# Performance work log

Hardware: AMD Instinct MI355X
Metric: run time of the kernel (lower is better)

## Reference

```python
import jax, jax.numpy as jnp
import numpy as np

D_MODEL = 32
N_HEADS = 4
D_K = 8
D_V = 8
LN_EPS = 1e-5
MASK_FILL = -1.0e9


def _layernorm(x, eps=LN_EPS):
    # torch.nn.LayerNorm with default affine params (gamma=1, beta=0)
    mu = jnp.mean(x, axis=-1, keepdims=True)
    var = jnp.var(x, axis=-1, keepdims=True)  # biased, matches torch
    return (x - mu) * jax.lax.rsqrt(var + eps)


def setup_inputs() -> dict:
    key = jax.random.key(0)
    ks = jax.random.split(key, 12)
    B, S = 8, 2048
    w = 1.0 / np.float32(np.sqrt(D_MODEL))
    return {
        "input_Q": jax.random.normal(ks[0], (B, S, D_MODEL), dtype=jnp.float32),
        "input_K": jax.random.normal(ks[1], (B, S, D_MODEL), dtype=jnp.float32),
        "input_V": jax.random.normal(ks[2], (B, S, D_MODEL), dtype=jnp.float32),
        "attn_mask": jax.random.randint(ks[3], (B, S, S), 0, 2).astype(jnp.bool_),
        "W_Q": jax.random.normal(ks[4], (D_MODEL, D_K * N_HEADS), dtype=jnp.float32) * w,
        "b_Q": jax.random.normal(ks[5], (D_K * N_HEADS,), dtype=jnp.float32) * 0.02,
        "W_K": jax.random.normal(ks[6], (D_MODEL, D_K * N_HEADS), dtype=jnp.float32) * w,
        "b_K": jax.random.normal(ks[7], (D_K * N_HEADS,), dtype=jnp.float32) * 0.02,
        "W_V": jax.random.normal(ks[8], (D_MODEL, D_V * N_HEADS), dtype=jnp.float32) * w,
        "b_V": jax.random.normal(ks[9], (D_V * N_HEADS,), dtype=jnp.float32) * 0.02,
        "W_O": jax.random.normal(ks[10], (D_V * N_HEADS, D_MODEL), dtype=jnp.float32) * w,
        "b_O": jax.random.normal(ks[11], (D_MODEL,), dtype=jnp.float32) * 0.02,
    }


def reference(input_Q, input_K, input_V, attn_mask, W_Q, b_Q, W_K, b_K, W_V, b_V, W_O, b_O):
    B, S, _ = input_Q.shape
    residual = input_Q
    # projections -> [B, H, S, d_head]
    Q = (input_Q @ W_Q + b_Q).reshape(B, S, N_HEADS, D_K).transpose(0, 2, 1, 3)
    K = (input_K @ W_K + b_K).reshape(B, S, N_HEADS, D_K).transpose(0, 2, 1, 3)
    V = (input_V @ W_V + b_V).reshape(B, S, N_HEADS, D_V).transpose(0, 2, 1, 3)
    scale = 1.0 / jnp.sqrt(jnp.asarray(D_K, dtype=Q.dtype))
    scores = jnp.einsum("bhqd,bhkd->bhqk", Q, K) * scale  # [B,H,S,S]
    scores = jnp.where(attn_mask[:, None, :, :], jnp.asarray(MASK_FILL, scores.dtype), scores)
    attn_ratio = jax.nn.softmax(scores, axis=-1)
    ctx = jnp.einsum("bhqk,bhkd->bhqd", attn_ratio, V)  # [B,H,S,Dv]
    self_attn = ctx.transpose(0, 2, 1, 3).reshape(B, S, N_HEADS * D_V)
    attn_output = self_attn @ W_O + b_O
    return (_layernorm(attn_output + residual), self_attn)
```

## Files before the change

### kernel.cpp

```cpp
#include <hip/hip_runtime.h>
#include <math.h>

#define D_MODEL 32
#define S_LEN   2048
#define B_SZ    8
#define NTOK    (B_SZ * S_LEN)
#define LN_EPS  1e-5f
#define LOG2E   1.44269504088896340736f
#define QK_SCALE 0.35355339059327373f
#define PROJ_BLKS (NTOK / 8)

typedef __attribute__((ext_vector_type(8)))  short    short8b;
typedef __attribute__((ext_vector_type(4)))  short    short4b;
typedef __attribute__((ext_vector_type(4)))  unsigned uint4v;
typedef __attribute__((ext_vector_type(16))) float    f32x16;

__device__ __forceinline__ unsigned short f2bf(float f) {
    unsigned u = __builtin_bit_cast(unsigned, f);
    unsigned r = (u + 0x7FFFu + ((u >> 16) & 1u)) >> 16;
    return (unsigned short)r;
}
__device__ __forceinline__ float bf2f(unsigned short h) {
    return __builtin_bit_cast(float, (unsigned)h << 16);
}
__device__ __forceinline__ unsigned cvtpk_bf16(float lo, float hi) {
    unsigned r;
    asm("v_cvt_pk_bf16_f32 %0, %1, %2" : "=v"(r) : "v"(lo), "v"(hi));
    return r;
}


__global__ __launch_bounds__(256) void prep_kernel(
    const float* __restrict__ xQ, const float* __restrict__ xK,
    const float* __restrict__ xV,
    const float* __restrict__ WQ, const float* __restrict__ bQ,
    const float* __restrict__ WK, const float* __restrict__ bK,
    const float* __restrict__ WV, const float* __restrict__ bV,
    unsigned short* __restrict__ QHC, unsigned short* __restrict__ QLC,
    unsigned short* __restrict__ KC,  unsigned short* __restrict__ VC)
{
    int bid = blockIdx.x;
    int t   = threadIdx.x;

    int which = bid / PROJ_BLKS;
    int xb    = bid - which * PROJ_BLKS;
    const float* x; const float* W; const float* bias; float scale;
    if (which == 0)      { x = xQ; W = WQ; bias = bQ; scale = QK_SCALE * LOG2E; }
    else if (which == 1) { x = xK; W = WK; bias = bK; scale = 1.0f; }
    else                 { x = xV; W = WV; bias = bV; scale = 1.0f; }

    __shared__ float xs[8][32];
    __shared__ float Ws[32][32];
    long base = (long)xb * 256;
    xs[t >> 5][t & 31] = x[base + t];
#pragma unroll
    for (int i = 0; i < 4; ++i) {
        int f = i * 256 + t;
        Ws[f >> 5][f & 31] = W[f];
    }
    __syncthreads();
    int r = t >> 5, j = t & 31;
    float acc = bias[j];
#pragma unroll
    for (int i = 0; i < 32; ++i) acc = fmaf(xs[r][i], Ws[i][j], acc);
    acc *= scale;

    long tok = (long)xb * 8 + r;
    long b   = tok >> 11;
    long ti  = tok & (S_LEN - 1);
    int  ch  = (int)(ti >> 5), kq = (int)(ti & 31);
    int  h   = j >> 3, d = j & 7;

    if (which == 0) {
        size_t qi = ((((size_t)b * 64 + ch) * 4 + h) * 32 + kq) * 8 + d;
        unsigned short hv = f2bf(acc);
        QHC[qi] = hv;
        QLC[qi] = f2bf(acc - bf2f(hv));
    } else if (which == 1) {
        size_t ki = (((((size_t)b * 64 + ch) * 4 + h) * 2 + 0) * 32 + kq) * 8 + d;
        unsigned short hv = f2bf(acc);
        KC[ki]       = hv;
        KC[ki + 256] = f2bf(acc - bf2f(hv));
    } else {
        size_t vi = (((size_t)b * 64 + ch) * 4 + h) * 256 + (size_t)d * 32 + kq;
        VC[vi] = f2bf(acc);
    }
}

__global__ __launch_bounds__(512, 4) void attn_fused_kernel(
    const unsigned short* __restrict__ QHC, const unsigned short* __restrict__ QLC,
    const unsigned short* __restrict__ KC,  const unsigned short* __restrict__ VC,
    const void* __restrict__ mask,
    const float* __restrict__ WO, const float* __restrict__ bO,
    const float* __restrict__ resid,
    float* __restrict__ sa_out, float* __restrict__ out0)
{
    constexpr int SEGLEN = 1024;
    constexpr int NPT    = SEGLEN / 64;
    __shared__ unsigned long long mpk[2][2][32][5];
    __shared__ float ctx_lds[2][32][33];
    __shared__ float l_lds[2][32][4];
    __shared__ float sa_lds[32][33];
    __shared__ float Ws[32][32];

    int raw  = blockIdx.x;
    int cid  = (raw & 7) * 64 + (raw >> 3);
    int b    = cid >> 6;
    int qt   = cid & 63;
    int tid  = threadIdx.x;
    int w    = tid >> 6;
    int h    = w & 3;
    int seg  = w >> 2;
    int lane = tid & 63;
    int q    = lane & 31;
    int half = lane >> 5;
    int tok0 = qt * 32;
    long tokbase = (long)b * S_LEN + tok0;
    long tokq    = tokbase + q;
    int k0   = seg * SEGLEN;
    int ch0  = k0 >> 5;

#pragma unroll
    for (int i = 0; i < 2; ++i) {
        int f = i * 512 + tid;
        Ws[f >> 5][f & 31] = WO[f];
    }

    int probe = ((const int*)mask)[lane];
    bool is32 = (__ballot((probe & ~0xFF) == 0) == ~0ULL);

    auto pack_group = [&](int g, int buf) {
#pragma unroll
        for (int i = 0; i < 4; ++i) {
            int r = (w << 2) + i;
            if (is32) {
                const int4* rp = (const int4*)((const int*)mask
                                               + (tokbase + r) * (long)S_LEN);
#pragma unroll
                for (int s2 = 0; s2 < 2; ++s2) {
                    int4 v = rp[s2 * 256 + g * 64 + lane];
                    unsigned long long b0 = __ballot(v.x != 0);
                    unsigned long long b1 = __ballot(v.y != 0);
                    unsigned long long b2 = __ballot(v.z != 0);
                    unsigned long long b3 = __ballot(v.w != 0);
                    if (lane == 0) {
                        mpk[buf][s2][r][0] = b0; mpk[buf][s2][r][1] = b1;
                        mpk[buf][s2][r][2] = b2; mpk[buf][s2][r][3] = b3;
                    }
                }
            } else {
                const int* rp = (const int*)((const unsigned char*)mask
                                             + (tokbase + r) * (long)S_LEN);
#pragma unroll
                for (int s2 = 0; s2 < 2; ++s2) {
                    int v = rp[s2 * 256 + g * 64 + lane];
                    unsigned long long b0 = __ballot((v & 0x000000FF) != 0);
                    unsigned long long b1 = __ballot((v & 0x0000FF00) != 0);
                    unsigned long long b2 = __ballot((v & 0x00FF0000) != 0);
                    unsigned long long b3 = __ballot((v & 0xFF000000u) != 0);
                    if (lane == 0) {
                        mpk[buf][s2][r][0] = b0; mpk[buf][s2][r][1] = b1;
                        mpk[buf][s2][r][2] = b2; mpk[buf][s2][r][3] = b3;
                    }
                }
            }
        }
    };

    f32x16 zero16;
#pragma unroll
    for (int i = 0; i < 16; ++i) zero16[i] = 0.0f;

    short ovv = (q == 8) ? (short)0x3F80 : (short)0;
    short8b ovf;
#pragma unroll
    for (int i = 0; i < 8; ++i) ovf[i] = ovv;

    size_t qoff = ((((size_t)b * 64 + qt) * 4 + h) * 32 + q) * 8;
    short8b qhf = *(const short8b*)(QHC + qoff);
    short8b qlf = *(const short8b*)(QLC + qoff);
    f32x16 cpv = zero16;

    const unsigned short* Kb0 = KC + (((size_t)b * 64) * 4 + h) * 512
                                   + (size_t)half * 256 + (size_t)q * 8;
    const unsigned short* Vb0 = VC + (((size_t)b * 64) * 4 + h) * 256
                                   + (size_t)q * 32 + half * 4;

    short8b kfA = *(const short8b*)(Kb0 + (size_t)ch0 * 2048);
    short8b kfB = *(const short8b*)(Kb0 + (size_t)(ch0 + 1) * 2048);
    short8b vf1c, vf2c;
    if (q < 8) {
        const unsigned short* vr = Vb0 + (size_t)ch0 * 1024;
        short4b a0 = *(const short4b*)(vr);
        short4b a1 = *(const short4b*)(vr + 8);
        short4b a2 = *(const short4b*)(vr + 16);
        short4b a3 = *(const short4b*)(vr + 24);
        vf1c = __builtin_shufflevector(a0, a1, 0, 1, 2, 3, 4, 5, 6, 7);
        vf2c = __builtin_shufflevector(a2, a3, 0, 1, 2, 3, 4, 5, 6, 7);
    } else { vf1c = ovf; vf2c = ovf; }

    pack_group(0, 0);
    __syncthreads();

#pragma unroll 1
    for (int g = 0; g < 4; ++g) {
        int cur = g & 1;

        if (g + 1 < 4) pack_group(g + 1, cur ^ 1);

        unsigned long long mg[4];
        mg[0] = mpk[cur][seg][q][0];
        mg[1] = mpk[cur][seg][q][1];
        mg[2] = mpk[cur][seg][q][2];
        mg[3] = mpk[cur][seg][q][3];

#pragma unroll 1
        for (int p = 0; p < 4; ++p) {
            int pa  = g * 4 + p;
            int chA = ch0 + 2 * pa;
            int chB = chA + 1;

            short8b kfA_n = kfA, kfB_n = kfB;
            if (pa + 1 < NPT) {
                kfA_n = *(const short8b*)(Kb0 + (size_t)(chA + 2) * 2048);
                kfB_n = *(const short8b*)(Kb0 + (size_t)(chB + 2) * 2048);
            }

            unsigned shA = (unsigned)(p * 16 + half);
            unsigned nA[4], nB[4];
#pragma unroll
            for (int c = 0; c < 4; ++c) {
                nA[c] = (unsigned)(mg[c] >> shA);
                nB[c] = (unsigned)(mg[c] >> (shA + 8u));
            }

            __builtin_amdgcn_s_setprio(1);
            f32x16 accA = __builtin_amdgcn_mfma_f32_32x32x16_bf16(kfA, qhf, zero16, 0, 0, 0);
            f32x16 accB = __builtin_amdgcn_mfma_f32_32x32x16_bf16(kfB, qhf, zero16, 0, 0, 0);
            accA = __builtin_amdgcn_mfma_f32_32x32x16_bf16(kfA, qlf, accA, 0, 0, 0);
            accB = __builtin_amdgcn_mfma_f32_32x32x16_bf16(kfB, qlf, accB, 0, 0, 0);
            __builtin_amdgcn_s_setprio(0);

            short8b vf1n, vf2n;
            if (q < 8) {
                const unsigned short* vr = Vb0 + (size_t)chB * 1024;
                short4b a0 = *(const short4b*)(vr);
                short4b a1 = *(const short4b*)(vr + 8);
                short4b a2 = *(const short4b*)(vr + 16);
                short4b a3 = *(const short4b*)(vr + 24);
                vf1n = __builtin_shufflevector(a0, a1, 0, 1, 2, 3, 4, 5, 6, 7);
                vf2n = __builtin_shufflevector(a2, a3, 0, 1, 2, 3, 4, 5, 6, 7);
            } else { vf1n = ovf; vf2n = ovf; }

            {
                unsigned pr[8];
#pragma unroll
                for (int j = 0; j < 8; ++j) {
                    const int c0 = (2 * j) & 3, c1 = (2 * j + 1) & 3;
                    const int s  = 2 * (j >> 1);
                    float p0 = ((nA[c0] >> s) & 1u) ? 0.0f
                             : __builtin_amdgcn_exp2f(accA[2 * j]);
                    float p1 = ((nA[c1] >> s) & 1u) ? 0.0f
                             : __builtin_amdgcn_exp2f(accA[2 * j + 1]);
                    pr[j] = cvtpk_bf16(p0, p1);
                }
                uint4v t1, t2;
                t1.x = pr[0]; t1.y = pr[1]; t1.z = pr[2]; t1.w = pr[3];
                t2.x = pr[4]; t2.y = pr[5]; t2.z = pr[6]; t2.w = pr[7];
                short8b pfa = __builtin_bit_cast(short8b, t1);
                short8b pfb = __builtin_bit_cast(short8b, t2);

                __builtin_amdgcn_s_setprio(1);
                cpv = __builtin_amdgcn_mfma_f32_32x32x16_bf16(vf1c, pfa, cpv, 0, 0, 0);
                cpv = __builtin_amdgcn_mfma_f32_32x32x16_bf16(vf2c, pfb, cpv, 0, 0, 0);
                __builtin_amdgcn_s_setprio(0);
            }

            short8b vf1nn, vf2nn;
            if (pa + 1 < NPT && q < 8) {
                const unsigned short* vr = Vb0 + (size_t)(chA + 2) * 1024;
                short4b a0 = *(const short4b*)(vr);
                short4b a1 = *(const short4b*)(vr + 8);
                short4b a2 = *(const short4b*)(vr + 16);
                short4b a3 = *(const short4b*)(vr + 24);
                vf1nn = __builtin_shufflevector(a0, a1, 0, 1, 2, 3, 4, 5, 6, 7);
                vf2nn = __builtin_shufflevector(a2, a3, 0, 1, 2, 3, 4, 5, 6, 7);
            } else { vf1nn = ovf; vf2nn = ovf; }

            {
                unsigned pr[8];
#pragma unroll
                for (int j = 0; j < 8; ++j) {
                    const int c0 = (2 * j) & 3, c1 = (2 * j + 1) & 3;
                    const int s  = 2 * (j >> 1);
                    float p0 = ((nB[c0] >> s) & 1u) ? 0.0f
                             : __builtin_amdgcn_exp2f(accB[2 * j]);
                    float p1 = ((nB[c1] >> s) & 1u) ? 0.0f
                             : __builtin_amdgcn_exp2f(accB[2 * j + 1]);
                    pr[j] = cvtpk_bf16(p0, p1);
                }
                uint4v t1, t2;
                t1.x = pr[0]; t1.y = pr[1]; t1.z = pr[2]; t1.w = pr[3];
                t2.x = pr[4]; t2.y = pr[5]; t2.z = pr[6]; t2.w = pr[7];
                short8b pfa = __builtin_bit_cast(short8b, t1);
                short8b pfb = __builtin_bit_cast(short8b, t2);

                __builtin_amdgcn_s_setprio(1);
                cpv = __builtin_amdgcn_mfma_f32_32x32x16_bf16(vf1n, pfa, cpv, 0, 0, 0);
                cpv = __builtin_amdgcn_mfma_f32_32x32x16_bf16(vf2n, pfb, cpv, 0, 0, 0);
                __builtin_amdgcn_s_setprio(0);
            }

            kfA = kfA_n;
            kfB = kfB_n;
            vf1c = vf1nn;
            vf2c = vf2nn;
        }

        __syncthreads();
    }

    ctx_lds[seg][q][h * 8 + half * 4 + 0] = cpv[0];
    ctx_lds[seg][q][h * 8 + half * 4 + 1] = cpv[1];
    ctx_lds[seg][q][h * 8 + half * 4 + 2] = cpv[2];
    ctx_lds[seg][q][h * 8 + half * 4 + 3] = cpv[3];
    if (half == 0) l_lds[seg][q][h] = cpv[4];
    __syncthreads();

    int r = (tid >> 5) & 15;
    int j = tid & 31;
#pragma unroll
    for (int pass = 0; pass < 2; ++pass) {
        int tok = pass * 16 + r;
        float L  = l_lds[0][tok][j >> 3] + l_lds[1][tok][j >> 3];
        float cx = ctx_lds[0][tok][j] + ctx_lds[1][tok][j];
        float sa = cx / L;
        sa_lds[tok][j] = sa;
        sa_out[(tokbase + tok) * 32 + j] = sa;
    }
    __syncthreads();

#pragma unroll
    for (int pass = 0; pass < 2; ++pass) {
        int tok = pass * 16 + r;
        long grow = (tokbase + tok) * 32;
        float y = bO[j] + resid[grow + j];
#pragma unroll
        for (int i = 0; i < 32; ++i) y = fmaf(sa_lds[tok][i], Ws[i][j], y);

        float sum = y;
#pragma unroll
        for (int o = 16; o >= 1; o >>= 1) sum += __shfl_xor(sum, o, 32);
        float mu = sum * (1.0f / 32.0f);
        float d  = y - mu;
        float sq = d * d;
#pragma unroll
        for (int o = 16; o >= 1; o >>= 1) sq += __shfl_xor(sq, o, 32);
        float var = sq * (1.0f / 32.0f);
        out0[grow + j] = d * rsqrtf(var + LN_EPS);
    }
}

extern "C" void kernel_launch(void* const* d_in, const int* in_sizes, int n_in,
                              void* d_out, int out_size, void* d_ws, size_t ws_size,
                              hipStream_t stream)
{
    const float* inQ = (const float*)d_in[0];
    const float* inK = (const float*)d_in[1];
    const float* inV = (const float*)d_in[2];
    const void*  mask = d_in[3];
    const float* WQ = (const float*)d_in[4];
    const float* bQ = (const float*)d_in[5];
    const float* WK = (const float*)d_in[6];
    const float* bK = (const float*)d_in[7];
    const float* WV = (const float*)d_in[8];
    const float* bV = (const float*)d_in[9];
    const float* WO = (const float*)d_in[10];
    const float* bO = (const float*)d_in[11];

    float* out0 = (float*)d_out;
    float* sa   = (float*)d_out + (long)NTOK * 32;

    char* ws = (char*)d_ws;
    unsigned short* QHC = (unsigned short*)(ws + 256);
    unsigned short* QLC = QHC + (size_t)NTOK * 32;
    unsigned short* KC  = QLC + (size_t)NTOK * 32;
    unsigned short* VC  = KC  + (size_t)NTOK * 64;

    prep_kernel<<<3 * PROJ_BLKS, 256, 0, stream>>>(
        inQ, inK, inV, WQ, bQ, WK, bK, WV, bV, QHC, QLC, KC, VC);

    attn_fused_kernel<<<B_SZ * 64, 512, 0, stream>>>(
        QHC, QLC, KC, VC, mask, WO, bO, inQ, sa, out0);
}
```

Baseline: 61.50 us.

## Split mask prefetch into issue/commit and unroll inner pair loop

Mask loads for the next group are now issued into registers at the start of a group. The ballot-and-LDS packing is deferred until after two of the four pair iterations, so global load latency overlaps with MFMA and exp work instead of stalling before compute. The inner loop over four pairs is also fully unrolled through a macro. This raises register pressure from the eight held int4 mask values and the larger unrolled code, which may reduce occupancy.

```diff
diff --git a/kernel.cpp b/kernel.cpp
--- a/kernel.cpp
+++ b/kernel.cpp
@@ -116,7 +116,6 @@
     int half = lane >> 5;
     int tok0 = qt * 32;
     long tokbase = (long)b * S_LEN + tok0;
-    long tokq    = tokbase + q;
     int k0   = seg * SEGLEN;
     int ch0  = k0 >> 5;
 
@@ -129,43 +128,56 @@
     int probe = ((const int*)mask)[lane];
     bool is32 = (__ballot((probe & ~0xFF) == 0) == ~0ULL);
 
-    auto pack_group = [&](int g, int buf) {
-#pragma unroll
-        for (int i = 0; i < 4; ++i) {
-            int r = (w << 2) + i;
-            if (is32) {
-                const int4* rp = (const int4*)((const int*)mask
-                                               + (tokbase + r) * (long)S_LEN);
-#pragma unroll
-                for (int s2 = 0; s2 < 2; ++s2) {
-                    int4 v = rp[s2 * 256 + g * 64 + lane];
-                    unsigned long long b0 = __ballot(v.x != 0);
-                    unsigned long long b1 = __ballot(v.y != 0);
-                    unsigned long long b2 = __ballot(v.z != 0);
-                    unsigned long long b3 = __ballot(v.w != 0);
-                    if (lane == 0) {
-                        mpk[buf][s2][r][0] = b0; mpk[buf][s2][r][1] = b1;
-                        mpk[buf][s2][r][2] = b2; mpk[buf][s2][r][3] = b3;
-                    }
-                }
-            } else {
-                const int* rp = (const int*)((const unsigned char*)mask
-                                             + (tokbase + r) * (long)S_LEN);
-#pragma unroll
-                for (int s2 = 0; s2 < 2; ++s2) {
-                    int v = rp[s2 * 256 + g * 64 + lane];
-                    unsigned long long b0 = __ballot((v & 0x000000FF) != 0);
-                    unsigned long long b1 = __ballot((v & 0x0000FF00) != 0);
-                    unsigned long long b2 = __ballot((v & 0x00FF0000) != 0);
-                    unsigned long long b3 = __ballot((v & 0xFF000000u) != 0);
-                    if (lane == 0) {
-                        mpk[buf][s2][r][0] = b0; mpk[buf][s2][r][1] = b1;
-                        mpk[buf][s2][r][2] = b2; mpk[buf][s2][r][3] = b3;
-                    }
-                }
-            }
-        }
-    };
+    long rb = tokbase + (w << 2);
+    const int4* r32_0 = (const int4*)((const int*)mask + (rb + 0) * (long)S_LEN);
+    const int4* r32_1 = (const int4*)((const int*)mask + (rb + 1) * (long)S_LEN);
+    const int4* r32_2 = (const int4*)((const int*)mask + (rb + 2) * (long)S_LEN);
+    const int4* r32_3 = (const int4*)((const int*)mask + (rb + 3) * (long)S_LEN);
+    const int* r8_0 = (const int*)((const unsigned char*)mask + (rb + 0) * (long)S_LEN);
+    const int* r8_1 = (const int*)((const unsigned char*)mask + (rb + 1) * (long)S_LEN);
+    const int* r8_2 = (const int*)((const unsigned char*)mask + (rb + 2) * (long)S_LEN);
+    const int* r8_3 = (const int*)((const unsigned char*)mask + (rb + 3) * (long)S_LEN);
+
+    int4 m0_0, m0_1, m1_0, m1_1, m2_0, m2_1, m3_0, m3_1;
+
+#define MASK_ISSUE(G)                                                        \
+    if (is32) {                                                              \
+        m0_0 = r32_0[(G) * 64 + lane]; m0_1 = r32_0[256 + (G) * 64 + lane];  \
+        m1_0 = r32_1[(G) * 64 + lane]; m1_1 = r32_1[256 + (G) * 64 + lane];  \
+        m2_0 = r32_2[(G) * 64 + lane]; m2_1 = r32_2[256 + (G) * 64 + lane];  \
+        m3_0 = r32_3[(G) * 64 + lane]; m3_1 = r32_3[256 + (G) * 64 + lane];  \
+    } else {                                                                 \
+        m0_0.x = r8_0[(G) * 64 + lane]; m0_1.x = r8_0[256 + (G) * 64 + lane];\
+        m1_0.x = r8_1[(G) * 64 + lane]; m1_1.x = r8_1[256 + (G) * 64 + lane];\
+        m2_0.x = r8_2[(G) * 64 + lane]; m2_1.x = r8_2[256 + (G) * 64 + lane];\
+        m3_0.x = r8_3[(G) * 64 + lane]; m3_1.x = r8_3[256 + (G) * 64 + lane];\
+    }
+
+#define CMT1(MV, RI, S2, BUF)                                                \
+    {                                                                        \
+        unsigned long long c0, c1, c2, c3;                                   \
+        if (is32) {                                                          \
+            c0 = __ballot((MV).x != 0); c1 = __ballot((MV).y != 0);          \
+            c2 = __ballot((MV).z != 0); c3 = __ballot((MV).w != 0);          \
+        } else {                                                             \
+            c0 = __ballot(((MV).x & 0x000000FF) != 0);                       \
+            c1 = __ballot(((MV).x & 0x0000FF00) != 0);                       \
+            c2 = __ballot(((MV).x & 0x00FF0000) != 0);                       \
+            c3 = __ballot(((MV).x & 0xFF000000u) != 0);                      \
+        }                                                                    \
+        if (lane == 0) {                                                     \
+            mpk[BUF][S2][(w << 2) + (RI)][0] = c0;                           \
+            mpk[BUF][S2][(w << 2) + (RI)][1] = c1;                           \
+            mpk[BUF][S2][(w << 2) + (RI)][2] = c2;                           \
+            mpk[BUF][S2][(w << 2) + (RI)][3] = c3;                           \
+        }                                                                    \
+    }
+
+#define MASK_COMMIT(BUF)                                                     \
+    CMT1(m0_0, 0, 0, BUF) CMT1(m0_1, 0, 1, BUF)                              \
+    CMT1(m1_0, 1, 0, BUF) CMT1(m1_1, 1, 1, BUF)                              \
+    CMT1(m2_0, 2, 0, BUF) CMT1(m2_1, 2, 1, BUF)                              \
+    CMT1(m3_0, 3, 0, BUF) CMT1(m3_1, 3, 1, BUF)
 
     f32x16 zero16;
 #pragma unroll
@@ -199,14 +211,105 @@
         vf2c = __builtin_shufflevector(a2, a3, 0, 1, 2, 3, 4, 5, 6, 7);
     } else { vf1c = ovf; vf2c = ovf; }
 
-    pack_group(0, 0);
+    MASK_ISSUE(0)
+    MASK_COMMIT(0)
     __syncthreads();
+
+#define PAIR_BODY(G, PP)                                                     \
+    {                                                                        \
+        int pa  = (G) * 4 + (PP);                                            \
+        int chA = ch0 + 2 * pa;                                              \
+        int chB = chA + 1;                                                   \
+        short8b kfA_n = kfA, kfB_n = kfB;                                    \
+        if (pa + 1 < NPT) {                                                  \
+            kfA_n = *(const short8b*)(Kb0 + (size_t)(chA + 2) * 2048);       \
+            kfB_n = *(const short8b*)(Kb0 + (size_t)(chB + 2) * 2048);       \
+        }                                                                    \
+        unsigned shA = (unsigned)((PP) * 16 + half);                         \
+        unsigned nA[4], nB[4];                                               \
+        _Pragma("unroll")                                                    \
+        for (int c = 0; c < 4; ++c) {                                        \
+            nA[c] = (unsigned)(mg[c] >> shA);                                \
+            nB[c] = (unsigned)(mg[c] >> (shA + 8u));                         \
+        }                                                                    \
+        __builtin_amdgcn_s_setprio(1);                                       \
+        f32x16 accA = __builtin_amdgcn_mfma_f32_32x32x16_bf16(kfA, qhf, zero16, 0, 0, 0); \
+        f32x16 accB = __builtin_amdgcn_mfma_f32_32x32x16_bf16(kfB, qhf, zero16, 0, 0, 0); \
+        accA = __builtin_amdgcn_mfma_f32_32x32x16_bf16(kfA, qlf, accA, 0, 0, 0); \
+        accB = __builtin_amdgcn_mfma_f32_32x32x16_bf16(kfB, qlf, accB, 0, 0, 0); \
+        __builtin_amdgcn_s_setprio(0);                                       \
+        short8b vf1n, vf2n;                                                  \
+        if (q < 8) {                                                         \
+            const unsigned short* vr = Vb0 + (size_t)chB * 1024;             \
+            short4b a0 = *(const short4b*)(vr);                              \
+            short4b a1 = *(const short4b*)(vr + 8);                          \
+            short4b a2 = *(const short4b*)(vr + 16);                         \
+            short4b a3 = *(const short4b*)(vr + 24);                         \
+            vf1n = __builtin_shufflevector(a0, a1, 0, 1, 2, 3, 4, 5, 6, 7);  \
+            vf2n = __builtin_shufflevector(a2, a3, 0, 1, 2, 3, 4, 5, 6, 7);  \
+        } else { vf1n = ovf; vf2n = ovf; }                                   \
+        {                                                                    \
+            unsigned pr[8];                                                  \
+            _Pragma("unroll")                                                \
+            for (int j2 = 0; j2 < 8; ++j2) {                                 \
+                const int c0 = (2 * j2) & 3, c1 = (2 * j2 + 1) & 3;          \
+                const int s  = 2 * (j2 >> 1);                                \
+                float p0 = ((nA[c0] >> s) & 1u) ? 0.0f                       \
+                         : __builtin_amdgcn_exp2f(accA[2 * j2]);             \
+                float p1 = ((nA[c1] >> s) & 1u) ? 0.0f                       \
+                         : __builtin_amdgcn_exp2f(accA[2 * j2 + 1]);         \
+                pr[j2] = cvtpk_bf16(p0, p1);                                 \
+            }                                                                \
+            uint4v t1, t2;                                                   \
+            t1.x = pr[0]; t1.y = pr[1]; t1.z = pr[2]; t1.w = pr[3];          \
+            t2.x = pr[4]; t2.y = pr[5]; t2.z = pr[6]; t2.w = pr[7];          \
+            short8b pfa = __builtin_bit_cast(short8b, t1);                   \
+            short8b pfb = __builtin_bit_cast(short8b, t2);                   \
+            __builtin_amdgcn_s_setprio(1);                                   \
+            cpv = __builtin_amdgcn_mfma_f32_32x32x16_bf16(vf1c, pfa, cpv, 0, 0, 0); \
+            cpv = __builtin_amdgcn_mfma_f32_32x32x16_bf16(vf2c, pfb, cpv, 0, 0, 0); \
+            __builtin_amdgcn_s_setprio(0);                                   \
+        }                                                                    \
+        short8b vf1nn, vf2nn;                                                \
+        if (pa + 1 < NPT && q < 8) {                                         \
+            const unsigned short* vr = Vb0 + (size_t)(chA + 2) * 1024;       \
+            short4b a0 = *(const short4b*)(vr);                              \
+            short4b a1 = *(const short4b*)(vr + 8);                          \
+            short4b a2 = *(const short4b*)(vr + 16);                         \
+            short4b a3 = *(const short4b*)(vr + 24);                         \
+            vf1nn = __builtin_shufflevector(a0, a1, 0, 1, 2, 3, 4, 5, 6, 7); \
+            vf2nn = __builtin_shufflevector(a2, a3, 0, 1, 2, 3, 4, 5, 6, 7); \
+        } else { vf1nn = ovf; vf2nn = ovf; }                                 \
+        {                                                                    \
+            unsigned pr[8];                                                  \
+            _Pragma("unroll")                                                \
+            for (int j2 = 0; j2 < 8; ++j2) {                                 \
+                const int c0 = (2 * j2) & 3, c1 = (2 * j2 + 1) & 3;          \
+                const int s  = 2 * (j2 >> 1);                                \
+                float p0 = ((nB[c0] >> s) & 1u) ? 0.0f                       \
+                         : __builtin_amdgcn_exp2f(accB[2 * j2]);             \
+                float p1 = ((nB[c1] >> s) & 1u) ? 0.0f                       \
+                         : __builtin_amdgcn_exp2f(accB[2 * j2 + 1]);         \
+                pr[j2] = cvtpk_bf16(p0, p1);                                 \
+            }                                                                \
+            uint4v t1, t2;                                                   \
+            t1.x = pr[0]; t1.y = pr[1]; t1.z = pr[2]; t1.w = pr[3];          \
+            t2.x = pr[4]; t2.y = pr[5]; t2.z = pr[6]; t2.w = pr[7];          \
+            short8b pfa = __builtin_bit_cast(short8b, t1);                   \
+            short8b pfb = __builtin_bit_cast(short8b, t2);                   \
+            __builtin_amdgcn_s_setprio(1);                                   \
+            cpv = __builtin_amdgcn_mfma_f32_32x32x16_bf16(vf1n, pfa, cpv, 0, 0, 0); \
+            cpv = __builtin_amdgcn_mfma_f32_32x32x16_bf16(vf2n, pfb, cpv, 0, 0, 0); \
+            __builtin_amdgcn_s_setprio(0);                                   \
+        }                                                                    \
+        kfA = kfA_n; kfB = kfB_n; vf1c = vf1nn; vf2c = vf2nn;                \
+    }
 
 #pragma unroll 1
     for (int g = 0; g < 4; ++g) {
         int cur = g & 1;
 
-        if (g + 1 < 4) pack_group(g + 1, cur ^ 1);
+        if (g + 1 < 4) { MASK_ISSUE(g + 1) }
 
         unsigned long long mg[4];
         mg[0] = mpk[cur][seg][q][0];
@@ -214,111 +317,20 @@
         mg[2] = mpk[cur][seg][q][2];
         mg[3] = mpk[cur][seg][q][3];
 
-#pragma unroll 1
-        for (int p = 0; p < 4; ++p) {
-            int pa  = g * 4 + p;
-            int chA = ch0 + 2 * pa;
-            int chB = chA + 1;
-
-            short8b kfA_n = kfA, kfB_n = kfB;
-            if (pa + 1 < NPT) {
-                kfA_n = *(const short8b*)(Kb0 + (size_t)(chA + 2) * 2048);
-                kfB_n = *(const short8b*)(Kb0 + (size_t)(chB + 2) * 2048);
-            }
-
-            unsigned shA = (unsigned)(p * 16 + half);
-            unsigned nA[4], nB[4];
-#pragma unroll
-            for (int c = 0; c < 4; ++c) {
-                nA[c] = (unsigned)(mg[c] >> shA);
-                nB[c] = (unsigned)(mg[c] >> (shA + 8u));
-            }
-
-            __builtin_amdgcn_s_setprio(1);
-            f32x16 accA = __builtin_amdgcn_mfma_f32_32x32x16_bf16(kfA, qhf, zero16, 0, 0, 0);
-            f32x16 accB = __builtin_amdgcn_mfma_f32_32x32x16_bf16(kfB, qhf, zero16, 0, 0, 0);
-            accA = __builtin_amdgcn_mfma_f32_32x32x16_bf16(kfA, qlf, accA, 0, 0, 0);
-            accB = __builtin_amdgcn_mfma_f32_32x32x16_bf16(kfB, qlf, accB, 0, 0, 0);
-            __builtin_amdgcn_s_setprio(0);
-
-            short8b vf1n, vf2n;
-            if (q < 8) {
-                const unsigned short* vr = Vb0 + (size_t)chB * 1024;
-                short4b a0 = *(const short4b*)(vr);
-                short4b a1 = *(const short4b*)(vr + 8);
-                short4b a2 = *(const short4b*)(vr + 16);
-                short4b a3 = *(const short4b*)(vr + 24);
-                vf1n = __builtin_shufflevector(a0, a1, 0, 1, 2, 3, 4, 5, 6, 7);
-                vf2n = __builtin_shufflevector(a2, a3, 0, 1, 2, 3, 4, 5, 6, 7);
-            } else { vf1n = ovf; vf2n = ovf; }
-
-            {
-                unsigned pr[8];
-#pragma unroll
-                for (int j = 0; j < 8; ++j) {
-                    const int c0 = (2 * j) & 3, c1 = (2 * j + 1) & 3;
-                    const int s  = 2 * (j >> 1);
-                    float p0 = ((nA[c0] >> s) & 1u) ? 0.0f
-                             : __builtin_amdgcn_exp2f(accA[2 * j]);
-                    float p1 = ((nA[c1] >> s) & 1u) ? 0.0f
-                             : __builtin_amdgcn_exp2f(accA[2 * j + 1]);
-                    pr[j] = cvtpk_bf16(p0, p1);
-                }
-                uint4v t1, t2;
-                t1.x = pr[0]; t1.y = pr[1]; t1.z = pr[2]; t1.w = pr[3];
-                t2.x = pr[4]; t2.y = pr[5]; t2.z = pr[6]; t2.w = pr[7];
-                short8b pfa = __builtin_bit_cast(short8b, t1);
-                short8b pfb = __builtin_bit_cast(short8b, t2);
-
-                __builtin_amdgcn_s_setprio(1);
-                cpv = __builtin_amdgcn_mfma_f32_32x32x16_bf16(vf1c, pfa, cpv, 0, 0, 0);
-                cpv = __builtin_amdgcn_mfma_f32_32x32x16_bf16(vf2c, pfb, cpv, 0, 0, 0);
-                __builtin_amdgcn_s_setprio(0);
-            }
-
-            short8b vf1nn, vf2nn;
-            if (pa + 1 < NPT && q < 8) {
-                const unsigned short* vr = Vb0 + (size_t)(chA + 2) * 1024;
-                short4b a0 = *(const short4b*)(vr);
-                short4b a1 = *(const short4b*)(vr + 8);
-                short4b a2 = *(const short4b*)(vr + 16);
-                short4b a3 = *(const short4b*)(vr + 24);
-                vf1nn = __builtin_shufflevector(a0, a1, 0, 1, 2, 3, 4, 5, 6, 7);
-                vf2nn = __builtin_shufflevector(a2, a3, 0, 1, 2, 3, 4, 5, 6, 7);
-            } else { vf1nn = ovf; vf2nn = ovf; }
-
-            {
-                unsigned pr[8];
-#pragma unroll
-                for (int j = 0; j < 8; ++j) {
-                    const int c0 = (2 * j) & 3, c1 = (2 * j + 1) & 3;
-                    const int s  = 2 * (j >> 1);
-                    float p0 = ((nB[c0] >> s) & 1u) ? 0.0f
-                             : __builtin_amdgcn_exp2f(accB[2 * j]);
-                    float p1 = ((nB[c1] >> s) & 1u) ? 0.0f
-                             : __builtin_amdgcn_exp2f(accB[2 * j + 1]);
-                    pr[j] = cvtpk_bf16(p0, p1);
-                }
-                uint4v t1, t2;
-                t1.x = pr[0]; t1.y = pr[1]; t1.z = pr[2]; t1.w = pr[3];
-                t2.x = pr[4]; t2.y = pr[5]; t2.z = pr[6]; t2.w = pr[7];
-                short8b pfa = __builtin_bit_cast(short8b, t1);
-                short8b pfb = __builtin_bit_cast(short8b, t2);
-
-                __builtin_amdgcn_s_setprio(1);
-                cpv = __builtin_amdgcn_mfma_f32_32x32x16_bf16(vf1n, pfa, cpv, 0, 0, 0);
-                cpv = __builtin_amdgcn_mfma_f32_32x32x16_bf16(vf2n, pfb, cpv, 0, 0, 0);
-                __builtin_amdgcn_s_setprio(0);
-            }
-
-            kfA = kfA_n;
-            kfB = kfB_n;
-            vf1c = vf1nn;
-            vf2c = vf2nn;
-        }
+        PAIR_BODY(g, 0)
+        PAIR_BODY(g, 1)
+
+        if (g + 1 < 4) { MASK_COMMIT(cur ^ 1) }
+
+        PAIR_BODY(g, 2)
+        PAIR_BODY(g, 3)
 
         __syncthreads();
     }
+#undef PAIR_BODY
+#undef MASK_COMMIT
+#undef CMT1
+#undef MASK_ISSUE
 
     ctx_lds[seg][q][h * 8 + half * 4 + 0] = cpv[0];
     ctx_lds[seg][q][h * 8 + half * 4 + 1] = cpv[1];
```

Measured after the change: 104.4 us. +69.8%, slower.
